# Kernel tuning notes

Hardware: AMD Instinct MI355X
Metric: run time of the kernel (lower is better)

The kernel has to match this reference:

```python
import jax, jax.numpy as jnp
import numpy as np

Q = 8       # number of spectral mixture components
NDIMS = 2   # input coordinate dimension
LATENT = 64
OUT = Q + Q + Q * NDIMS  # 32


def _mlp(p, W1, b1, W2, b2):
    # eqx.nn.MLP(depth=1): Linear -> selu -> Linear -> softplus
    h = jax.nn.selu(p @ W1.T + b1)
    return jax.nn.softplus(h @ W2.T + b2)


def _feats(p, W1, b1, W2, b2):
    # Precompute per-point features ONCE (fixes the per-pair MLP recompute).
    a = _mlp(p, W1, b1, W2, b2)                      # [N, OUT]
    w = a[:, :Q]                                     # mixture weights  [N, Q]
    s = a[:, Q:2 * Q]                                # lengthscales     [N, Q]
    f = a[:, 2 * Q:].reshape(-1, Q, NDIMS)           # frequencies      [N, Q, D]
    phi = jnp.einsum('nqd,nd->nq', f, p)             # f @ p per point  [N, Q]
    return w, s, phi


def setup_inputs() -> dict:
    key = jax.random.key(0)
    ks = jax.random.split(key, 6)
    N = 2048
    x = jax.random.normal(ks[0], (N, NDIMS), jnp.float32)
    y = jax.random.normal(ks[1], (N, NDIMS), jnp.float32)
    W1 = jax.random.normal(ks[2], (LATENT, NDIMS), jnp.float32) / np.sqrt(NDIMS).astype(np.float32)
    b1 = jax.random.normal(ks[3], (LATENT,), jnp.float32) * 0.1
    W2 = jax.random.normal(ks[4], (OUT, LATENT), jnp.float32) / np.sqrt(LATENT).astype(np.float32)
    b2 = jax.random.normal(ks[5], (OUT,), jnp.float32) * 0.1
    return {"x": x, "y": y, "W1": W1, "b1": b1, "W2": W2, "b2": b2}


def reference(x, y, W1, b1, W2, b2):
    # Original: k_xy = vmap(vmap(eval,(0,None)),(None,0))(Y, X)
    #   => output[i, j] = eval(x=Y[j], y=X[i]), shape [Nx, Ny].
    # A* features come from the X argument (eval's `y` role),
    # B* features come from the Y argument (eval's `x` role).
    wA, sA, phiA = _feats(x, W1, b1, W2, b2)   # [Nx, Q]
    wB, sB, phiB = _feats(y, W1, b1, W2, b2)   # [Ny, Q]

    d2 = jnp.sum((x[:, None, :] - y[None, :, :]) ** 2, axis=-1)      # [Nx, Ny]
    s2 = sA[:, None, :] ** 2 + sB[None, :, :] ** 2                   # [Nx, Ny, Q]
    gibbs = jnp.sqrt(2.0 * sA[:, None, :] * sB[None, :, :]) / s2 * jnp.exp(-d2[:, :, None] / s2)
    cosine = jnp.cos(2.0 * jnp.pi * (phiB[None, :, :] - phiA[:, None, :]))
    return jnp.sum(wA[:, None, :] * wB[None, :, :] * gibbs * cosine, axis=-1)  # [Nx, Ny]
```

## Files before the change

### kernel.cpp

```cpp
#include <hip/hip_runtime.h>
#include <math.h>

#define QN 8
#define NDIMS 2
#define LATENT 64
#define OUTC 32
#define IT 16

__global__ __launch_bounds__(256) void feat_kernel(
    const float* __restrict__ x, const float* __restrict__ y, int n,
    const float* __restrict__ W1, const float* __restrict__ b1,
    const float* __restrict__ W2, const float* __restrict__ b2,
    float* __restrict__ featX, float* __restrict__ featY)
{
    const int t    = blockIdx.x * 256 + threadIdx.x;
    const int pt   = t >> 5;
    const int o    = t & 31;
    const int npts = 2 * n;
    if (pt >= npts) return;

    const float* p = (pt < n) ? (x + 2 * pt) : (y + 2 * (pt - n));
    float p0 = p[0], p1 = p[1];

    const float kScale = 1.0507009873554804934193349852946f;
    const float kAlpha = 1.6732632423543772848170429916717f;

    const float4* w2v = (const float4*)(W2 + o * LATENT);
    float z0 = b2[o], z1 = 0.f, z2 = 0.f, z3 = 0.f;
    #pragma unroll
    for (int c = 0; c < LATENT / 16; ++c) {
        float hb[16];
        #pragma unroll
        for (int r = 0; r < 16; ++r) {
            int k = 16 * c + r;
            float zz = fmaf(W1[2 * k], p0, fmaf(W1[2 * k + 1], p1, b1[k]));
            hb[r] = kScale * (zz > 0.f ? zz : kAlpha * (__expf(zz) - 1.f));
        }
        float4 w0 = w2v[4 * c + 0];
        float4 w1v = w2v[4 * c + 1];
        float4 w2q = w2v[4 * c + 2];
        float4 w3 = w2v[4 * c + 3];
        z0 = fmaf(w0.x,  hb[0],  fmaf(w0.y,  hb[1],  fmaf(w0.z,  hb[2],  fmaf(w0.w,  hb[3],  z0))));
        z1 = fmaf(w1v.x, hb[4],  fmaf(w1v.y, hb[5],  fmaf(w1v.z, hb[6],  fmaf(w1v.w, hb[7],  z1))));
        z2 = fmaf(w2q.x, hb[8],  fmaf(w2q.y, hb[9],  fmaf(w2q.z, hb[10], fmaf(w2q.w, hb[11], z2))));
        z3 = fmaf(w3.x,  hb[12], fmaf(w3.y,  hb[13], fmaf(w3.z,  hb[14], fmaf(w3.w,  hb[15], z3))));
    }
    float z = (z0 + z1) + (z2 + z3);
    float av = fmaxf(z, 0.f) + __logf(1.f + __expf(-fabsf(z)));

    const int lane = threadIdx.x & 63;
    const int base = lane & 32;
    const int q    = lane & 7;
    float w_ = __shfl(av, base + q, 64);
    float s_ = __shfl(av, base + 8 + q, 64);
    float f0 = __shfl(av, base + 16 + 2 * q, 64);
    float f1 = __shfl(av, base + 17 + 2 * q, 64);

    if ((lane & 31) < 8) {
        const float TWO_PI  = 6.283185307179586f;
        const float ROOT4_2 = 1.18920711500272107f;
        float phi = fmaf(f0, p0, f1 * p1);
        float rr  = phi - floorf(phi);
        float ang = TWO_PI * rr;
        float* fo = (pt < n) ? (featX + 32 * pt) : (featY + 32 * (pt - n));
        fo[q]          = w_ * sqrtf(s_) * ROOT4_2;
        fo[QN + q]     = s_ * s_;
        fo[2 * QN + q] = __cosf(ang);
        fo[3 * QN + q] = __sinf(ang);
    }
}

__global__ __launch_bounds__(256) void pair_kernel(
    const float* __restrict__ x, const float* __restrict__ y, int n,
    const float* __restrict__ fA, const float* __restrict__ fB,
    float* __restrict__ out)
{
    __shared__ __align__(16) float faS[IT * 32];
    __shared__ __align__(16) float xaS[IT * 2];

    const int tid = threadIdx.x;
    const int j   = blockIdx.x * 256 + tid;
    const int i0  = blockIdx.y * IT;

    if (tid < IT * 8) {
        ((float4*)faS)[tid] = ((const float4*)(fA + (size_t)i0 * 32))[tid];
    } else if (tid < IT * 8 + IT / 2) {
        ((float4*)xaS)[tid - IT * 8] = ((const float4*)(x + 2 * i0))[tid - IT * 8];
    }
    __syncthreads();

    if (j >= n) return;

    const float4* fb4 = (const float4*)(fB + 32 * j);
    float4 fu0 = fb4[0], fu1 = fb4[1];
    float4 fs0 = fb4[2], fs1 = fb4[3];
    float4 fc0 = fb4[4], fc1 = fb4[5];
    float4 fn0 = fb4[6], fn1 = fb4[7];
    float uB[QN]  = {fu0.x,fu0.y,fu0.z,fu0.w, fu1.x,fu1.y,fu1.z,fu1.w};
    float ssB[QN] = {fs0.x,fs0.y,fs0.z,fs0.w, fs1.x,fs1.y,fs1.z,fs1.w};
    float cB[QN]  = {fc0.x,fc0.y,fc0.z,fc0.w, fc1.x,fc1.y,fc1.z,fc1.w};
    float snB[QN] = {fn0.x,fn0.y,fn0.z,fn0.w, fn1.x,fn1.y,fn1.z,fn1.w};

    float2 yv = *(const float2*)(y + 2 * j);
    const float LOG2E = 1.4426950408889634f;

    #pragma unroll 2
    for (int ii = 0; ii < IT; ++ii) {
        int i = i0 + ii;
        if (i >= n) break;

        const float4* fa4 = (const float4*)(faS + ii * 32);
        float4 au0 = fa4[0], au1 = fa4[1];
        float4 as0 = fa4[2], as1 = fa4[3];
        float4 ac0 = fa4[4], ac1 = fa4[5];
        float4 an0 = fa4[6], an1 = fa4[7];
        float uA[QN]  = {au0.x,au0.y,au0.z,au0.w, au1.x,au1.y,au1.z,au1.w};
        float ssA[QN] = {as0.x,as0.y,as0.z,as0.w, as1.x,as1.y,as1.z,as1.w};
        float cA[QN]  = {ac0.x,ac0.y,ac0.z,ac0.w, ac1.x,ac1.y,ac1.z,ac1.w};
        float snA[QN] = {an0.x,an0.y,an0.z,an0.w, an1.x,an1.y,an1.z,an1.w};

        float dx  = xaS[2 * ii]     - yv.x;
        float dy  = xaS[2 * ii + 1] - yv.y;
        float d2l = fmaf(dx, dx, dy * dy) * LOG2E;

        float acc = 0.f;
        #pragma unroll
        for (int q = 0; q < QN; ++q) {
            float s2  = ssA[q] + ssB[q];
            float inv = __builtin_amdgcn_rcpf(s2);
            float e   = __builtin_amdgcn_exp2f(-d2l * inv);
            float g   = uA[q] * uB[q] * inv * e;
            float c   = fmaf(cA[q], cB[q], snA[q] * snB[q]);
            acc = fmaf(g, c, acc);
        }
        out[(long)i * n + j] = acc;
    }
}

extern "C" void kernel_launch(void* const* d_in, const int* in_sizes, int n_in,
                              void* d_out, int out_size, void* d_ws, size_t ws_size,
                              hipStream_t stream)
{
    const float* x  = (const float*)d_in[0];
    const float* y  = (const float*)d_in[1];
    const float* W1 = (const float*)d_in[2];
    const float* b1 = (const float*)d_in[3];
    const float* W2 = (const float*)d_in[4];
    const float* b2 = (const float*)d_in[5];
    float* out = (float*)d_out;

    int n = in_sizes[0] / NDIMS;

    float* featX = (float*)d_ws;
    float* featY = featX + (size_t)n * 32;

    int npts = 2 * n;
    int featThreads = npts * OUTC;
    hipLaunchKernelGGL(feat_kernel, dim3((featThreads + 255) / 256), dim3(256), 0, stream,
                       x, y, n, W1, b1, W2, b2, featX, featY);

    dim3 grid((n + 255) / 256, (n + IT - 1) / IT);
    hipLaunchKernelGGL(pair_kernel, grid, dim3(256), 0, stream,
                       x, y, n, featX, featY, out);
}
```

Before: 27.91 us.

## Compute four output columns per thread in pair kernel with float4 stores

Each thread now handles four consecutive j columns, keeping their B features in registers and reusing each LDS-loaded A row across all four. Output is written as one float4 store per row, and the row tile shrinks from 16 to 8. The aim is to cut LDS traffic per output and widen global stores. The cost is much higher register pressure, since 128 B-feature floats are held per thread, which may lower occupancy. There is also no tail handling when n is not a multiple of 4.

```diff
diff --git a/kernel.cpp b/kernel.cpp
--- a/kernel.cpp
+++ b/kernel.cpp
@@ -5,7 +5,8 @@
 #define NDIMS 2
 #define LATENT 64
 #define OUTC 32
-#define IT 16
+#define IT 8
+#define JPT 4
 
 __global__ __launch_bounds__(256) void feat_kernel(
     const float* __restrict__ x, const float* __restrict__ y, int n,
@@ -79,7 +80,6 @@
     __shared__ __align__(16) float xaS[IT * 2];
 
     const int tid = threadIdx.x;
-    const int j   = blockIdx.x * 256 + tid;
     const int i0  = blockIdx.y * IT;
 
     if (tid < IT * 8) {
@@ -89,20 +89,29 @@
     }
     __syncthreads();
 
-    if (j >= n) return;
+    const int j0 = blockIdx.x * (256 * JPT) + tid * JPT;
+    if (j0 >= n) return;
 
-    const float4* fb4 = (const float4*)(fB + 32 * j);
-    float4 fu0 = fb4[0], fu1 = fb4[1];
-    float4 fs0 = fb4[2], fs1 = fb4[3];
-    float4 fc0 = fb4[4], fc1 = fb4[5];
-    float4 fn0 = fb4[6], fn1 = fb4[7];
-    float uB[QN]  = {fu0.x,fu0.y,fu0.z,fu0.w, fu1.x,fu1.y,fu1.z,fu1.w};
-    float ssB[QN] = {fs0.x,fs0.y,fs0.z,fs0.w, fs1.x,fs1.y,fs1.z,fs1.w};
-    float cB[QN]  = {fc0.x,fc0.y,fc0.z,fc0.w, fc1.x,fc1.y,fc1.z,fc1.w};
-    float snB[QN] = {fn0.x,fn0.y,fn0.z,fn0.w, fn1.x,fn1.y,fn1.z,fn1.w};
+    float uB[JPT][QN], ssB[JPT][QN], cB[JPT][QN], snB[JPT][QN];
+    float yj0[JPT], yj1[JPT];
+    #pragma unroll
+    for (int jj = 0; jj < JPT; ++jj) {
+        const float4* fb4 = (const float4*)(fB + 32 * (j0 + jj));
+        float4 a0 = fb4[0], a1 = fb4[1], a2 = fb4[2], a3 = fb4[3];
+        float4 a4 = fb4[4], a5 = fb4[5], a6 = fb4[6], a7 = fb4[7];
+        uB[jj][0]=a0.x; uB[jj][1]=a0.y; uB[jj][2]=a0.z; uB[jj][3]=a0.w;
+        uB[jj][4]=a1.x; uB[jj][5]=a1.y; uB[jj][6]=a1.z; uB[jj][7]=a1.w;
+        ssB[jj][0]=a2.x; ssB[jj][1]=a2.y; ssB[jj][2]=a2.z; ssB[jj][3]=a2.w;
+        ssB[jj][4]=a3.x; ssB[jj][5]=a3.y; ssB[jj][6]=a3.z; ssB[jj][7]=a3.w;
+        cB[jj][0]=a4.x; cB[jj][1]=a4.y; cB[jj][2]=a4.z; cB[jj][3]=a4.w;
+        cB[jj][4]=a5.x; cB[jj][5]=a5.y; cB[jj][6]=a5.z; cB[jj][7]=a5.w;
+        snB[jj][0]=a6.x; snB[jj][1]=a6.y; snB[jj][2]=a6.z; snB[jj][3]=a6.w;
+        snB[jj][4]=a7.x; snB[jj][5]=a7.y; snB[jj][6]=a7.z; snB[jj][7]=a7.w;
+        float2 yv = *(const float2*)(y + 2 * (j0 + jj));
+        yj0[jj] = yv.x; yj1[jj] = yv.y;
+    }
 
-    float2 yv = *(const float2*)(y + 2 * j);
-    const float LOG2E = 1.4426950408889634f;
+    const float NLOG2E = -1.4426950408889634f;
 
     #pragma unroll 2
     for (int ii = 0; ii < IT; ++ii) {
@@ -110,30 +119,39 @@
         if (i >= n) break;
 
         const float4* fa4 = (const float4*)(faS + ii * 32);
-        float4 au0 = fa4[0], au1 = fa4[1];
-        float4 as0 = fa4[2], as1 = fa4[3];
-        float4 ac0 = fa4[4], ac1 = fa4[5];
-        float4 an0 = fa4[6], an1 = fa4[7];
-        float uA[QN]  = {au0.x,au0.y,au0.z,au0.w, au1.x,au1.y,au1.z,au1.w};
-        float ssA[QN] = {as0.x,as0.y,as0.z,as0.w, as1.x,as1.y,as1.z,as1.w};
-        float cA[QN]  = {ac0.x,ac0.y,ac0.z,ac0.w, ac1.x,ac1.y,ac1.z,ac1.w};
-        float snA[QN] = {an0.x,an0.y,an0.z,an0.w, an1.x,an1.y,an1.z,an1.w};
+        float4 b0 = fa4[0], b1v = fa4[1], b2v = fa4[2], b3 = fa4[3];
+        float4 b4 = fa4[4], b5 = fa4[5], b6 = fa4[6], b7 = fa4[7];
+        float uA[QN]  = {b0.x,b0.y,b0.z,b0.w, b1v.x,b1v.y,b1v.z,b1v.w};
+        float ssA[QN] = {b2v.x,b2v.y,b2v.z,b2v.w, b3.x,b3.y,b3.z,b3.w};
+        float cA[QN]  = {b4.x,b4.y,b4.z,b4.w, b5.x,b5.y,b5.z,b5.w};
+        float snA[QN] = {b6.x,b6.y,b6.z,b6.w, b7.x,b7.y,b7.z,b7.w};
+        float xi0 = xaS[2 * ii], xi1 = xaS[2 * ii + 1];
 
-        float dx  = xaS[2 * ii]     - yv.x;
-        float dy  = xaS[2 * ii + 1] - yv.y;
-        float d2l = fmaf(dx, dx, dy * dy) * LOG2E;
+        float d2ln[JPT];
+        #pragma unroll
+        for (int jj = 0; jj < JPT; ++jj) {
+            float dx = xi0 - yj0[jj];
+            float dy = xi1 - yj1[jj];
+            d2ln[jj] = fmaf(dx, dx, dy * dy) * NLOG2E;
+        }
 
-        float acc = 0.f;
+        float4 accv;
+        float* accp = &accv.x;
         #pragma unroll
-        for (int q = 0; q < QN; ++q) {
-            float s2  = ssA[q] + ssB[q];
-            float inv = __builtin_amdgcn_rcpf(s2);
-            float e   = __builtin_amdgcn_exp2f(-d2l * inv);
-            float g   = uA[q] * uB[q] * inv * e;
-            float c   = fmaf(cA[q], cB[q], snA[q] * snB[q]);
-            acc = fmaf(g, c, acc);
+        for (int jj = 0; jj < JPT; ++jj) {
+            float acc = 0.f;
+            #pragma unroll
+            for (int q = 0; q < QN; ++q) {
+                float s2  = ssA[q] + ssB[jj][q];
+                float inv = __builtin_amdgcn_rcpf(s2);
+                float e   = __builtin_amdgcn_exp2f(d2ln[jj] * inv);
+                float t   = uA[q] * uB[jj][q];
+                float c   = fmaf(cA[q], cB[jj][q], snA[q] * snB[jj][q]);
+                acc = fmaf(t * inv * e, c, acc);
+            }
+            accp[jj] = acc;
         }
-        out[(long)i * n + j] = acc;
+        *(float4*)(out + (long)i * n + j0) = accv;
     }
 }
 
@@ -159,7 +177,7 @@
     hipLaunchKernelGGL(feat_kernel, dim3((featThreads + 255) / 256), dim3(256), 0, stream,
                        x, y, n, W1, b1, W2, b2, featX, featY);
 
-    dim3 grid((n + 255) / 256, (n + IT - 1) / IT);
+    dim3 grid((n + 256 * JPT - 1) / (256 * JPT), (n + IT - 1) / IT);
     hipLaunchKernelGGL(pair_kernel, grid, dim3(256), 0, stream,
                        x, y, n, featX, featY, out);
 }
```

Result: slower. 28.92 us (+3.6%).
